# Optimization experiments

Hardware: AMD Instinct MI355X
Metric: run time of the kernel (lower is better)

Reference implementation:

```python
import jax, jax.numpy as jnp
import numpy as np

N_NODES = 8192
N_FEAT = 256
N_EDGES = 131072
K = 4


def setup_inputs() -> dict:
    key = jax.random.key(0)
    k1, k2, k3 = jax.random.split(key, 3)
    x = jax.random.normal(k1, (N_NODES, N_FEAT), dtype=jnp.float32)
    edge_index = jax.random.randint(k2, (2, N_EDGES), 0, N_NODES, dtype=jnp.int64)
    edge_weight = jax.random.uniform(k3, (N_EDGES,), dtype=jnp.float32)
    return {"k": K, "x": x, "edge_index": edge_index, "edge_weight": edge_weight}


def reference(k, x, edge_index, edge_weight):
    n = x.shape[0]
    src, dst = edge_index[0], edge_index[1]
    # Symmetrized dense adjacency, matching the torch loop:
    #   adj[src, dst] = w  then  adj[dst, src] += w
    adj = jnp.zeros((n, n), dtype=x.dtype)
    adj = adj.at[src, dst].set(edge_weight)
    adj = adj.at[dst, src].add(edge_weight)
    # M = [I | A | A^2 | ... | A^{k-1}] (N x kN) times block_diag(x,...,x)
    # (kN x kF) is exactly concat([A^j @ x for j in 0..k-1], axis=1) -- we
    # compute that directly and never form the block-diagonal zeros.
    outs = [x]
    h = x
    for _ in range(1, k):
        h = adj @ h  # A^j @ x  (A symmetric, so order is immaterial)
        outs.append(h)
    return jnp.concatenate(outs, axis=1)  # [N, k*F]
```

## Files before the change

### kernel.cpp

```cpp
#include <hip/hip_runtime.h>

#define N_NODES 8192
#define N_FEAT  256
#define N_EDGES 131072
#define KPOW    4
#define OUT_LD  1024
#define RCAP    128
#define COL_MASK 8191u

typedef float    f32x4 __attribute__((ext_vector_type(4)));
typedef unsigned u32x4 __attribute__((ext_vector_type(4)));
typedef unsigned u32x2 __attribute__((ext_vector_type(2)));

#define EB 512

static __device__ __forceinline__ float bflo(unsigned u) {
    union { unsigned i; float f; } v; v.i = u << 16; return v.f;
}
static __device__ __forceinline__ float bfhi(unsigned u) {
    union { unsigned i; float f; } v; v.i = u & 0xffff0000u; return v.f;
}
static __device__ __forceinline__ unsigned short f2bf(float f) {
    union { float f; unsigned i; } v = { f };
    return (unsigned short)((v.i + 0x7fffu + ((v.i >> 16) & 1u)) >> 16);
}

__global__ void k_scatter_copy(const int* __restrict__ ei, const float* __restrict__ ew,
                               unsigned* __restrict__ len, u32x2* __restrict__ ent,
                               const float* __restrict__ x, float* __restrict__ out,
                               unsigned short* __restrict__ xb) {
    if (blockIdx.x < EB) {
        int e = blockIdx.x * blockDim.x + threadIdx.x;
        unsigned base = len[N_NODES];
        int src = __builtin_nontemporal_load(ei + e);
        int dst = __builtin_nontemporal_load(ei + N_EDGES + e);
        unsigned wbits = __float_as_uint(__builtin_nontemporal_load(ew + e));
        unsigned s0 = atomicAdd(&len[dst], 1u);
        unsigned s1 = atomicAdd(&len[src], 1u);
        s0 -= base; s1 -= base;
        if (s0 < RCAP) {
            u32x2 v; v.x = (unsigned)src; v.y = wbits;
            ent[(size_t)dst * RCAP + s0] = v;
        }
        if (s1 < RCAP) {
            u32x2 v; v.x = (1u << 30) | ((unsigned)e << 13) | (unsigned)dst; v.y = wbits;
            ent[(size_t)src * RCAP + s1] = v;
        }
    } else {
        int t = (blockIdx.x - EB) * blockDim.x + threadIdx.x;
        int row = t >> 6;
        int lane = t & 63;
        f32x4 v = __builtin_nontemporal_load((const f32x4*)(x + (size_t)row * N_FEAT + lane * 4));
        __builtin_nontemporal_store(v, (f32x4*)(out + (size_t)row * OUT_LD + lane * 4));
        u32x2 pb;
        pb.x = ((unsigned)f2bf(v.y) << 16) | f2bf(v.x);
        pb.y = ((unsigned)f2bf(v.w) << 16) | f2bf(v.z);
        __builtin_nontemporal_store(pb, (u32x2*)(xb + (size_t)row * N_FEAT + lane * 4));
    }
}

__global__ __launch_bounds__(256) void k_spmm(const unsigned* __restrict__ len,
                                              const u32x2* ent,
                                              u32x2* entw,
                                              const unsigned short* __restrict__ hinb,
                                              float* __restrict__ hout,
                                              unsigned short* __restrict__ houtb,
                                              int write_bf, int dedup) {
    __shared__ u32x2 sent[4 * RCAP];
    int wave = threadIdx.x >> 6;
    int lane = threadIdx.x & 63;
    int row = blockIdx.x * 4 + wave;
    unsigned base = len[N_NODES];
    unsigned un = len[row] - base;
    int n = __builtin_amdgcn_readfirstlane((int)(un > RCAP ? RCAP : un));

    const u32x2* ep = ent + (size_t)row * RCAP;
    u32x2* sp = sent + wave * RCAP;
    u32x2 e0 = __builtin_nontemporal_load(ep + lane);
    if (lane >= n) { e0.x = 0u; e0.y = 0u; }
    u32x2 e1; e1.x = 0u; e1.y = 0u;
    bool two = (n > 64);
    if (two) {
        e1 = __builtin_nontemporal_load(ep + 64 + lane);
        if (lane + 64 >= n) { e1.x = 0u; e1.y = 0u; }
    }

    if (dedup) {
        unsigned v0 = e0.x, v1 = e1.x;
        bool k0 = false, k1 = false;
        int j0 = n < 64 ? n : 64;
        for (int j = 0; j < j0; ++j) {
            unsigned b = (unsigned)__shfl((int)v0, j);
            if (b >> 30) {
                k0 |= (((b ^ v0) & COL_MASK) == 0u) && (b > v0);
                k1 |= (((b ^ v1) & COL_MASK) == 0u) && (b > v1);
            }
        }
        for (int j = 0; j < n - 64; ++j) {
            unsigned b = (unsigned)__shfl((int)v1, j);
            if (b >> 30) {
                k0 |= (((b ^ v0) & COL_MASK) == 0u) && (b > v0);
                k1 |= (((b ^ v1) & COL_MASK) == 0u) && (b > v1);
            }
        }
        u32x2 zz; zz.x = 0u; zz.y = 0u;
        u32x2* wrow = entw + (size_t)row * RCAP;
        if (lane < n && k0 && (v0 >> 30)) {
            e0 = zz; wrow[lane] = zz;
        }
        int s1 = lane + 64;
        if (two && s1 < n && k1 && (v1 >> 30)) {
            e1 = zz; wrow[s1] = zz;
        }
    }

    sp[lane] = e0;
    if (two) sp[lane + 64] = e1;
    __builtin_amdgcn_s_waitcnt(0);

    int half = lane >> 5;
    int fl   = lane & 31;
    const unsigned short* hbase = hinb + fl * 8;
    float a0 = 0.f, a1 = 0.f, a2 = 0.f, a3 = 0.f,
          a4 = 0.f, a5 = 0.f, a6 = 0.f, a7 = 0.f;
    int ng = (n + 15) >> 4;

    for (int g = 0; g < ng; ++g) {
        const u32x2* ge = sp + g * 16 + half;
        u32x4 us[8];
#pragma unroll
        for (int t = 0; t < 8; ++t) {
            unsigned c = ge[2 * t].x & COL_MASK;
            us[t] = *(const u32x4*)(hbase + (size_t)c * N_FEAT);
        }
#pragma unroll
        for (int t = 0; t < 8; ++t) {
            float w = __uint_as_float(ge[2 * t].y);
            a0 += w * bflo(us[t].x); a1 += w * bfhi(us[t].x);
            a2 += w * bflo(us[t].y); a3 += w * bfhi(us[t].y);
            a4 += w * bflo(us[t].z); a5 += w * bfhi(us[t].z);
            a6 += w * bflo(us[t].w); a7 += w * bfhi(us[t].w);
        }
    }

    a0 += __shfl_xor(a0, 32); a1 += __shfl_xor(a1, 32);
    a2 += __shfl_xor(a2, 32); a3 += __shfl_xor(a3, 32);
    a4 += __shfl_xor(a4, 32); a5 += __shfl_xor(a5, 32);
    a6 += __shfl_xor(a6, 32); a7 += __shfl_xor(a7, 32);

    if (half == 0) {
        float* op = hout + (size_t)row * OUT_LD + fl * 8;
        f32x4 r0; r0.x = a0; r0.y = a1; r0.z = a2; r0.w = a3;
        f32x4 r1; r1.x = a4; r1.y = a5; r1.z = a6; r1.w = a7;
        __builtin_nontemporal_store(r0, (f32x4*)op);
        __builtin_nontemporal_store(r1, (f32x4*)(op + 4));
    } else if (write_bf) {
        u32x4 pb;
        pb.x = ((unsigned)f2bf(a1) << 16) | f2bf(a0);
        pb.y = ((unsigned)f2bf(a3) << 16) | f2bf(a2);
        pb.z = ((unsigned)f2bf(a5) << 16) | f2bf(a4);
        pb.w = ((unsigned)f2bf(a7) << 16) | f2bf(a6);
        __builtin_nontemporal_store(pb, (u32x4*)(houtb + (size_t)row * N_FEAT + fl * 8));
    }
}

extern "C" void kernel_launch(void* const* d_in, const int* in_sizes, int n_in,
                              void* d_out, int out_size, void* d_ws, size_t ws_size,
                              hipStream_t stream) {
    const float* x  = (const float*)d_in[1];
    const int*   ei = (const int*)d_in[2];
    const float* ew = (const float*)d_in[3];
    float* out = (float*)d_out;

    unsigned* len = (unsigned*)d_ws;
    u32x2* ent = (u32x2*)(len + N_NODES + 64);
    unsigned short* hb0 = (unsigned short*)(ent + (size_t)N_NODES * RCAP);
    unsigned short* hb1 = hb0 + (size_t)N_NODES * N_FEAT;
    unsigned short* hb2 = hb1 + (size_t)N_NODES * N_FEAT;

    const int TB = 256;

    k_scatter_copy<<<EB + 2048, TB, 0, stream>>>(ei, ew, len, ent, x, out, hb0);

    const unsigned short* hin = hb0;
    for (int j = 1; j < KPOW; ++j) {
        float* hout = out + (size_t)j * N_FEAT;
        unsigned short* houtb = (j == 1) ? hb1 : hb2;
        int write_bf = (j < KPOW - 1) ? 1 : 0;
        int dedup    = (j == 1) ? 1 : 0;
        k_spmm<<<N_NODES / 4, TB, 0, stream>>>(len, ent, ent, hin,
                                               hout, houtb, write_bf, dedup);
        hin = houtb;
    }
}
```

Measured before the change: 129.7 us.

## Add feature-sliced SpMM kernel for second and third propagation hops

The first hop keeps the original per-row kernel, now specialised to always deduplicate and always write the bf16 copy. Hops two and three use a new kernel that splits the 256 features into four 64-wide slices across blocks. Each wave handles four rows and spreads eight edges across lane groups, with entries broadcast by shuffles instead of staged through shared memory. The goal is to keep each gathered slice of the input resident in cache and to raise parallelism, at the cost of re-reading edge lists four times and doing extra shuffle reductions.

```diff
diff --git a/kernel.cpp b/kernel.cpp
--- a/kernel.cpp
+++ b/kernel.cpp
@@ -64,8 +64,7 @@
                                               u32x2* entw,
                                               const unsigned short* __restrict__ hinb,
                                               float* __restrict__ hout,
-                                              unsigned short* __restrict__ houtb,
-                                              int write_bf, int dedup) {
+                                              unsigned short* __restrict__ houtb) {
     __shared__ u32x2 sent[4 * RCAP];
     int wave = threadIdx.x >> 6;
     int lane = threadIdx.x & 63;
@@ -85,7 +84,7 @@
         if (lane + 64 >= n) { e1.x = 0u; e1.y = 0u; }
     }
 
-    if (dedup) {
+    {
         unsigned v0 = e0.x, v1 = e1.x;
         bool k0 = false, k1 = false;
         int j0 = n < 64 ? n : 64;
@@ -154,13 +153,95 @@
         f32x4 r1; r1.x = a4; r1.y = a5; r1.z = a6; r1.w = a7;
         __builtin_nontemporal_store(r0, (f32x4*)op);
         __builtin_nontemporal_store(r1, (f32x4*)(op + 4));
-    } else if (write_bf) {
+    } else {
         u32x4 pb;
         pb.x = ((unsigned)f2bf(a1) << 16) | f2bf(a0);
         pb.y = ((unsigned)f2bf(a3) << 16) | f2bf(a2);
         pb.z = ((unsigned)f2bf(a5) << 16) | f2bf(a4);
         pb.w = ((unsigned)f2bf(a7) << 16) | f2bf(a6);
         __builtin_nontemporal_store(pb, (u32x4*)(houtb + (size_t)row * N_FEAT + fl * 8));
+    }
+}
+
+__global__ __launch_bounds__(256) void k_spmm_sliced(const unsigned* __restrict__ len,
+                                                     const u32x2* __restrict__ ent,
+                                                     const unsigned short* __restrict__ hinb,
+                                                     float* __restrict__ hout,
+                                                     unsigned short* __restrict__ houtb,
+                                                     int write_bf) {
+    int slice = blockIdx.x & 3;
+    int rgrp  = blockIdx.x >> 2;
+    int wave = threadIdx.x >> 6;
+    int lane = threadIdx.x & 63;
+    int es = lane >> 3;
+    int q  = lane & 7;
+    unsigned base = len[N_NODES];
+    const unsigned short* hsl = hinb + slice * 64 + q * 8;
+
+    for (int r = 0; r < 4; ++r) {
+        int row = rgrp * 16 + wave * 4 + r;
+        unsigned un = len[row] - base;
+        int n = __builtin_amdgcn_readfirstlane((int)(un > RCAP ? RCAP : un));
+        const u32x2* ep = ent + (size_t)row * RCAP;
+        u32x2 e0 = __builtin_nontemporal_load(ep + lane);
+        if (lane >= n) { e0.x = 0u; e0.y = 0u; }
+
+        float a0 = 0.f, a1 = 0.f, a2 = 0.f, a3 = 0.f,
+              a4 = 0.f, a5 = 0.f, a6 = 0.f, a7 = 0.f;
+        int ng  = (n + 7) >> 3;
+        int ng0 = ng < 8 ? ng : 8;
+        for (int g = 0; g < ng0; ++g) {
+            unsigned cx = (unsigned)__shfl((int)e0.x, g * 8 + es);
+            unsigned wb = (unsigned)__shfl((int)e0.y, g * 8 + es);
+            unsigned c = cx & COL_MASK;
+            u32x4 us = *(const u32x4*)(hsl + (size_t)c * N_FEAT);
+            float w = __uint_as_float(wb);
+            a0 += w * bflo(us.x); a1 += w * bfhi(us.x);
+            a2 += w * bflo(us.y); a3 += w * bfhi(us.y);
+            a4 += w * bflo(us.z); a5 += w * bfhi(us.z);
+            a6 += w * bflo(us.w); a7 += w * bfhi(us.w);
+        }
+        if (n > 64) {
+            u32x2 e1 = __builtin_nontemporal_load(ep + 64 + lane);
+            if (lane + 64 >= n) { e1.x = 0u; e1.y = 0u; }
+            for (int g = 8; g < ng; ++g) {
+                unsigned cx = (unsigned)__shfl((int)e1.x, (g - 8) * 8 + es);
+                unsigned wb = (unsigned)__shfl((int)e1.y, (g - 8) * 8 + es);
+                unsigned c = cx & COL_MASK;
+                u32x4 us = *(const u32x4*)(hsl + (size_t)c * N_FEAT);
+                float w = __uint_as_float(wb);
+                a0 += w * bflo(us.x); a1 += w * bfhi(us.x);
+                a2 += w * bflo(us.y); a3 += w * bfhi(us.y);
+                a4 += w * bflo(us.z); a5 += w * bfhi(us.z);
+                a6 += w * bflo(us.w); a7 += w * bfhi(us.w);
+            }
+        }
+
+        a0 += __shfl_xor(a0, 8); a0 += __shfl_xor(a0, 16); a0 += __shfl_xor(a0, 32);
+        a1 += __shfl_xor(a1, 8); a1 += __shfl_xor(a1, 16); a1 += __shfl_xor(a1, 32);
+        a2 += __shfl_xor(a2, 8); a2 += __shfl_xor(a2, 16); a2 += __shfl_xor(a2, 32);
+        a3 += __shfl_xor(a3, 8); a3 += __shfl_xor(a3, 16); a3 += __shfl_xor(a3, 32);
+        a4 += __shfl_xor(a4, 8); a4 += __shfl_xor(a4, 16); a4 += __shfl_xor(a4, 32);
+        a5 += __shfl_xor(a5, 8); a5 += __shfl_xor(a5, 16); a5 += __shfl_xor(a5, 32);
+        a6 += __shfl_xor(a6, 8); a6 += __shfl_xor(a6, 16); a6 += __shfl_xor(a6, 32);
+        a7 += __shfl_xor(a7, 8); a7 += __shfl_xor(a7, 16); a7 += __shfl_xor(a7, 32);
+
+        if (es == 0) {
+            float* op = hout + (size_t)row * OUT_LD + slice * 64 + q * 8;
+            f32x4 r0; r0.x = a0; r0.y = a1; r0.z = a2; r0.w = a3;
+            f32x4 r1; r1.x = a4; r1.y = a5; r1.z = a6; r1.w = a7;
+            __builtin_nontemporal_store(r0, (f32x4*)op);
+            __builtin_nontemporal_store(r1, (f32x4*)(op + 4));
+            if (write_bf) {
+                u32x4 pb;
+                pb.x = ((unsigned)f2bf(a1) << 16) | f2bf(a0);
+                pb.y = ((unsigned)f2bf(a3) << 16) | f2bf(a2);
+                pb.z = ((unsigned)f2bf(a5) << 16) | f2bf(a4);
+                pb.w = ((unsigned)f2bf(a7) << 16) | f2bf(a6);
+                __builtin_nontemporal_store(pb,
+                    (u32x4*)(houtb + (size_t)row * N_FEAT + slice * 64 + q * 8));
+            }
+        }
     }
 }
 
@@ -182,14 +263,11 @@
 
     k_scatter_copy<<<EB + 2048, TB, 0, stream>>>(ei, ew, len, ent, x, out, hb0);
 
-    const unsigned short* hin = hb0;
-    for (int j = 1; j < KPOW; ++j) {
-        float* hout = out + (size_t)j * N_FEAT;
-        unsigned short* houtb = (j == 1) ? hb1 : hb2;
-        int write_bf = (j < KPOW - 1) ? 1 : 0;
-        int dedup    = (j == 1) ? 1 : 0;
-        k_spmm<<<N_NODES / 4, TB, 0, stream>>>(len, ent, ent, hin,
-                                               hout, houtb, write_bf, dedup);
-        hin = houtb;
-    }
-}
+    k_spmm<<<N_NODES / 4, TB, 0, stream>>>(len, ent, ent, hb0,
+                                           out + N_FEAT, hb1);
+
+    k_spmm_sliced<<<4 * (N_NODES / 16), TB, 0, stream>>>(len, ent, hb1,
+                                                         out + 2 * N_FEAT, hb2, 1);
+    k_spmm_sliced<<<4 * (N_NODES / 16), TB, 0, stream>>>(len, ent, hb2,
+                                                         out + 3 * N_FEAT, (unsigned short*)0, 0);
+}
```

Result: slower. 152.2 us (+17.3%).
